# Performance work log

Measured on AMD Instinct MI355X. Metric: run time of the kernel, lower is better.

## Reference

```python
import jax, jax.numpy as jnp
import numpy as np

K = 76          # model dim = 6 + 30 + 30 + 10 (concat of modality embeddings)
H = 8           # heads; per-head dim == K (wide attention variant)
D = 6           # depth
T = 1024        # seq_length (frames)
B = 8           # batch
C = 2           # num_classes
EPS = 1e-5


def setup_inputs() -> dict:
    key = jax.random.key(0)
    ks = jax.random.split(key, 24)
    rn = lambda k, shape, s=0.02: (jax.random.normal(k, shape, jnp.float32) * s)
    return {
        # forward inputs (per-frame multimodal features)
        "v": jax.random.normal(ks[0], (B, T, 6), jnp.float32),
        "x": jax.random.normal(ks[1], (B, T, 137), jnp.float32),
        "y": jax.random.normal(ks[2], (B, T, 113), jnp.float32),
        "z": jax.random.normal(ks[3], (B, T, 35), jnp.float32),
        # modality embed linears (stored (in, out); torch does x @ W.T)
        "W_hp": rn(ks[4], (6, 6)),     "b_hp": jnp.zeros((6,), jnp.float32),
        "W_lm": rn(ks[5], (137, 30)),  "b_lm": jnp.zeros((30,), jnp.float32),
        "W_el": rn(ks[6], (113, 30)),  "b_el": jnp.zeros((30,), jnp.float32),
        "W_au": rn(ks[7], (35, 10)),   "b_au": jnp.zeros((10,), jnp.float32),
        "pos_emb": rn(ks[8], (T, K)),
        # per-block params stacked over depth for lax.scan
        "Wq": rn(ks[9], (D, K, H * K)),
        "Wk": rn(ks[10], (D, K, H * K)),
        "Wv": rn(ks[11], (D, K, H * K)),
        "Wu": rn(ks[12], (D, H * K, K)), "bu": jnp.zeros((D, K), jnp.float32),
        "ln1_s": jnp.ones((D, K), jnp.float32), "ln1_b": jnp.zeros((D, K), jnp.float32),
        "W1": rn(ks[13], (D, K, 4 * K)), "b1": jnp.zeros((D, 4 * K), jnp.float32),
        "W2": rn(ks[14], (D, 4 * K, K)), "b2": jnp.zeros((D, K), jnp.float32),
        "ln2_s": jnp.ones((D, K), jnp.float32), "ln2_b": jnp.zeros((D, K), jnp.float32),
        "W_out": rn(ks[15], (K, C)), "b_out": jnp.zeros((C,), jnp.float32),
    }


def _layernorm(h, s, b):
    mu = jnp.mean(h, axis=-1, keepdims=True)
    var = jnp.mean(jnp.square(h - mu), axis=-1, keepdims=True)
    return (h - mu) * jax.lax.rsqrt(var + EPS) * s + b


def reference(v, x, y, z,
              W_hp, b_hp, W_lm, b_lm, W_el, b_el, W_au, b_au,
              pos_emb, Wq, Wk, Wv, Wu, bu, ln1_s, ln1_b,
              W1, b1, W2, b2, ln2_s, ln2_b, W_out, b_out):
    b, t = v.shape[0], v.shape[1]
    tokens = jnp.concatenate([
        v @ W_hp + b_hp,
        x @ W_lm + b_lm,
        y @ W_el + b_el,
        z @ W_au + b_au,
    ], axis=2)                                   # (b, t, K)
    h = tokens + pos_emb[None, :, :]
    scale = 1.0 / np.sqrt(K)                     # dot / sqrt(e), e == k

    def block(hh, p):
        wq, wk, wv, wu, bu_, l1s, l1b, w1, b1_, w2, b2_, l2s, l2b = p
        # (b, t, H*K) -> (b, H, t, K); per-head dim is full K here
        q = (hh @ wq).reshape(b, t, H, K).transpose(0, 2, 1, 3)
        k_ = (hh @ wk).reshape(b, t, H, K).transpose(0, 2, 1, 3)
        vv = (hh @ wv).reshape(b, t, H, K).transpose(0, 2, 1, 3)
        dot = jax.nn.softmax(jnp.einsum('bhte,bhse->bhts', q, k_) * scale, axis=-1)
        att = jnp.einsum('bhts,bhse->bhte', dot, vv)        # (b, H, t, K)
        att = att.transpose(0, 2, 1, 3).reshape(b, t, H * K)
        att = att @ wu + bu_                                # unify heads -> (b, t, K)
        h1 = _layernorm(att + hh, l1s, l1b)
        ff = jax.nn.relu(h1 @ w1 + b1_) @ w2 + b2_
        return _layernorm(ff + h1, l2s, l2b), None

    h, _ = jax.lax.scan(
        block, h,
        (Wq, Wk, Wv, Wu, bu, ln1_s, ln1_b, W1, b1, W2, b2, ln2_s, ln2_b))
    return h @ W_out + b_out                     # (b, t, num_classes)
```

## Files before the change

### kernel.cpp

```cpp
#include <hip/hip_runtime.h>
#include <hip/hip_bf16.h>
#include <math.h>

#define B_   8
#define T_   1024
#define K_   76
#define KP_  96
#define H_   8
#define D_   6
#define C_   2
#define HK_  608
#define QKLD_ 640
#define FF_  304
#define FFP_ 320
#define EK_  320
#define BT_  8192
#define EPS_ 1e-5f
#define SCL2_ (0.11470786693528088f * 1.4426950408889634f)

typedef unsigned short u16;
typedef unsigned int u32;
typedef short bf16x8 __attribute__((ext_vector_type(8)));
typedef float f32x4 __attribute__((ext_vector_type(4)));

__device__ __forceinline__ u16 f2b(float f) {
  __hip_bfloat16 h = __float2bfloat16(f);
  return *reinterpret_cast<u16*>(&h);
}
__device__ __forceinline__ float b2f(u16 u) {
  __hip_bfloat16 h = *reinterpret_cast<__hip_bfloat16*>(&u);
  return __bfloat162float(h);
}
__device__ __forceinline__ u32 pack2(float a, float b) {
  __hip_bfloat162 t = __float22bfloat162_rn(make_float2(a, b));
  return *reinterpret_cast<u32*>(&t);
}

#define PER_L_ 304128ULL
__global__ __launch_bounds__(256) void wconv_kernel(
    const float* __restrict__ Wq, const float* __restrict__ Wk, const float* __restrict__ Wv,
    const float* __restrict__ Wu, const float* __restrict__ W1, const float* __restrict__ W2,
    u16* __restrict__ WT) {
  __shared__ float Ls[32][65];
  int zz = blockIdx.y;
  int d = zz / 6, wt = zz % 6;
  const float* in; int Kd, Nsrc, Nalloc, Kp; u16* out;
  size_t lb = (size_t)d * PER_L_;
  switch (wt) {
    case 0: in = Wq + (size_t)d*K_*HK_; Kd=K_;  Nsrc=HK_; Nalloc=640; Kp=KP_;  out = WT + lb;          break;
    case 1: in = Wk + (size_t)d*K_*HK_; Kd=K_;  Nsrc=HK_; Nalloc=640; Kp=KP_;  out = WT + lb + 61440;  break;
    case 2: in = Wv + (size_t)d*K_*HK_; Kd=K_;  Nsrc=HK_; Nalloc=640; Kp=KP_;  out = WT + lb + 122880; break;
    case 3: in = Wu + (size_t)d*HK_*K_; Kd=HK_; Nsrc=K_;  Nalloc=96;  Kp=HK_;  out = WT + lb + 184320; break;
    case 4: in = W1 + (size_t)d*K_*FF_; Kd=K_;  Nsrc=FF_; Nalloc=320; Kp=KP_;  out = WT + lb + 242688; break;
    default:in = W2 + (size_t)d*FF_*K_; Kd=FF_; Nsrc=K_;  Nalloc=96;  Kp=FFP_; out = WT + lb + 273408; break;
  }
  int tiles_k = Kp / 32;
  int tiles_n = (Nalloc + 63) / 64;
  int tile = blockIdx.x;
  if (tile >= tiles_k * tiles_n) return;
  int tn = tile / tiles_k, tk = tile % tiles_k;
  int n0 = tn * 64, k0 = tk * 32;
  for (int i = threadIdx.x; i < 2048; i += 256) {
    int kk = i >> 6, nn = i & 63;
    int gk = k0 + kk, gn = n0 + nn;
    int srccol = gn;
    if (wt < 3) {
      int hh8 = gn / 80, ft = gn - hh8 * 80;
      srccol = (ft < 76) ? (hh8 * 76 + ft) : -1;
    }
    Ls[kk][nn] = (gk < Kd && srccol >= 0 && srccol < Nsrc) ? in[(size_t)gk * Nsrc + srccol] : 0.f;
  }
  __syncthreads();
  for (int i = threadIdx.x; i < 2048; i += 256) {
    int nn = i >> 5, kk = i & 31;
    int gn = n0 + nn;
    if (gn < Nalloc) out[(size_t)gn * Kp + k0 + kk] = f2b(Ls[kk][nn]);
  }
}

__global__ void wembed_kernel(const float* __restrict__ W_hp, const float* __restrict__ b_hp,
                              const float* __restrict__ W_lm, const float* __restrict__ b_lm,
                              const float* __restrict__ W_el, const float* __restrict__ b_el,
                              const float* __restrict__ W_au, const float* __restrict__ b_au,
                              u16* __restrict__ WE) {
  int idx = blockIdx.x * 256 + threadIdx.x;
  if (idx >= 96 * EK_) return;
  int n = idx / EK_, kk = idx % EK_;
  float val = 0.f;
  if (n < 76) {
    if (kk < 6) { if (n < 6) val = W_hp[kk * 6 + n]; }
    else if (kk < 143) { int i = kk - 6; if (n >= 6 && n < 36) val = W_lm[i * 30 + (n - 6)]; }
    else if (kk < 256) { int i = kk - 143; if (n >= 36 && n < 66) val = W_el[i * 30 + (n - 36)]; }
    else if (kk < 291) { int i = kk - 256; if (n >= 66) val = W_au[i * 10 + (n - 66)]; }
    else if (kk == 291) {
      val = (n < 6) ? b_hp[n] : (n < 36) ? b_lm[n - 6] : (n < 66) ? b_el[n - 36] : b_au[n - 66];
    }
  }
  WE[idx] = f2b(val);
}

__global__ void pack_kernel(const float* __restrict__ v, const float* __restrict__ x,
                            const float* __restrict__ y, const float* __restrict__ z,
                            u16* __restrict__ xin) {
  int idx = blockIdx.x * 256 + threadIdx.x;
  if (idx >= BT_ * (EK_ / 2)) return;
  int bt = idx / (EK_ / 2), dc = idx % (EK_ / 2);
  int c0 = dc * 2;
  auto fetch = [&](int c) -> float {
    if (c < 6) return v[bt * 6 + c];
    if (c < 143) return x[bt * 137 + c - 6];
    if (c < 256) return y[bt * 113 + c - 143];
    if (c < 291) return z[bt * 35 + c - 256];
    if (c == 291) return 1.0f;
    return 0.f;
  };
  ((u32*)xin)[idx] = pack2(fetch(c0), fetch(c0 + 1));
}

template<int RT, int CT, int KSTEPS, int RELU, int LNFUSE, int TPB>
__global__ __launch_bounds__(TPB) void gemm_kernel(
    const u16* __restrict__ A, int lda,
    const u16* __restrict__ Wt, int ldw, unsigned long long wstride,
    const float* __restrict__ bias,
    u16* __restrict__ Cc, int ldc, int N,
    int ksplit, int klen, unsigned long long osplit,
    float cs,
    u16* __restrict__ vbt,
    const float* __restrict__ pos,
    const u16* __restrict__ res,
    const float* __restrict__ lns,
    const float* __restrict__ lnb) {
  __shared__ u16 Bs[CT * 16 * 56];
  const int tid = threadIdx.x;
  const int w = tid >> 6, lane = tid & 63;
  const int r = lane & 15, g = lane >> 4;
  const int n0 = blockIdx.x * CT * 16;
  const int m0 = blockIdx.y * (TPB / 64) * 16 * RT;
  const int z = blockIdx.z;
  const int k0 = z * ksplit;
  const int kend = k0 + klen;
  const u16* Wz = Wt + (size_t)z * wstride;
  const float* bias_eff = (z == 0) ? bias : nullptr;
  const float csz = (z == 0) ? cs : 1.f;
  u16* Cz = Cc + (size_t)z * osplit;
  constexpr int NB = (CT * 64 + TPB - 1) / TPB;

  const f32x4 fz = {0.f, 0.f, 0.f, 0.f};
  f32x4 acc[RT][CT];
  #pragma unroll
  for (int rt = 0; rt < RT; rt++)
    #pragma unroll
    for (int ct = 0; ct < CT; ct++) acc[rt][ct] = fz;

  bf16x8 a_all[RT][KSTEPS];
  #pragma unroll
  for (int rt = 0; rt < RT; rt++) {
    const u16* arow = A + (size_t)(m0 + (w * RT + rt) * 16 + r) * lda;
    #pragma unroll
    for (int ks = 0; ks < KSTEPS; ks++) {
      int kA = k0 + ks * 32 + g * 8;
      if (kA < kend) a_all[rt][ks] = *(const bf16x8*)(arow + kA);
      else a_all[rt][ks] = bf16x8{0, 0, 0, 0, 0, 0, 0, 0};
    }
  }

  uint4 bpre[NB];
  auto loadB = [&](int ks) {
    int kk = k0 + ks * 32;
    #pragma unroll
    for (int i0 = 0; i0 < NB; i0++) {
      int idx = tid + i0 * TPB;
      bpre[i0] = make_uint4(0, 0, 0, 0);
      if (idx < CT * 64) {
        int nn = idx >> 2, kc = idx & 3;
        if (kk + kc * 8 < kend)
          bpre[i0] = *(const uint4*)(Wz + (size_t)(n0 + nn) * ldw + kk + kc * 8);
      }
    }
  };
  loadB(0);

  for (int ks = 0; ks < KSTEPS; ks++) {
    __syncthreads();
    #pragma unroll
    for (int i0 = 0; i0 < NB; i0++) {
      int idx = tid + i0 * TPB;
      if (idx < CT * 64) {
        int nn = idx >> 2, kc = idx & 3;
        *(uint4*)&Bs[nn * 56 + (((kc ^ (nn & 3)) << 3))] = bpre[i0];
      }
    }
    __syncthreads();
    if (ks + 1 < KSTEPS) loadB(ks + 1);
    #pragma unroll
    for (int ct = 0; ct < CT; ct++) {
      bf16x8 bb = *(const bf16x8*)&Bs[(ct * 16 + r) * 56 + (((g ^ (r & 3)) << 3))];
      #pragma unroll
      for (int rt = 0; rt < RT; rt++)
        acc[rt][ct] = __builtin_amdgcn_mfma_f32_16x16x32_bf16(a_all[rt][ks], bb, acc[rt][ct], 0, 0, 0);
    }
  }

  if (LNFUSE) {
    #pragma unroll
    for (int reg = 0; reg < 4; reg++) {
      int row = m0 + w * 16 + g * 4 + reg;
      const u16* resr = res + (size_t)row * KP_;
      float vals[CT];
      float s = 0.f, s2 = 0.f;
      #pragma unroll
      for (int ct = 0; ct < CT; ct++) {
        int col = ct * 16 + r;
        float val = 0.f;
        if (col < N) {
          val = acc[0][ct][reg] + bias[col] + b2f(resr[col]);
          s += val; s2 += val * val;
        }
        vals[ct] = val;
      }
      #pragma unroll
      for (int m = 1; m < 16; m <<= 1) { s += __shfl_xor(s, m); s2 += __shfl_xor(s2, m); }
      float mu = s * (1.f / 76.f);
      float rstd = rsqrtf(s2 * (1.f / 76.f) - mu * mu + EPS_);
      u16* outr = Cz + (size_t)row * ldc;
      #pragma unroll
      for (int ct = 0; ct < CT; ct++) {
        int col = ct * 16 + r;
        u16 ov = 0;
        if (col < N) ov = f2b((vals[ct] - mu) * rstd * lns[col] + lnb[col]);
        if (col < ldc) outr[col] = ov;
      }
    }
  } else if (vbt && z == 2) {
    #pragma unroll
    for (int rt = 0; rt < RT; rt++) {
      #pragma unroll
      for (int ct = 0; ct < CT; ct++) {
        int feat = ct * 16 + r;
        int token = m0 + (w * RT + rt) * 16 + g * 4;
        int bb_ = token >> 10, tt = token & 1023;
        ushort4 pk;
        if (feat < 76) {
          pk.x = f2b(acc[rt][ct][0]); pk.y = f2b(acc[rt][ct][1]);
          pk.z = f2b(acc[rt][ct][2]); pk.w = f2b(acc[rt][ct][3]);
        } else {
          pk = make_ushort4(0, 0, 0, 0);
        }
        *(ushort4*)(vbt + (((size_t)(bb_ * 8 + blockIdx.x) * 80 + feat) << 10) + tt) = pk;
      }
    }
  } else {
    #pragma unroll
    for (int rt = 0; rt < RT; rt++) {
      #pragma unroll
      for (int ct = 0; ct < CT; ct++) {
        int col = n0 + ct * 16 + r;
        if (col < ldc) {
          #pragma unroll
          for (int reg = 0; reg < 4; reg++) {
            int row = m0 + (w * RT + rt) * 16 + g * 4 + reg;
            float val = acc[rt][ct][reg] * csz;
            if (bias_eff && col < N) val += bias_eff[col];
            if (pos && col < N) val += pos[(row & (T_ - 1)) * K_ + col];
            if (RELU) val = fmaxf(val, 0.f);
            Cz[(size_t)row * ldc + col] = f2b(val);
          }
        }
      }
    }
  }
}

__global__ __launch_bounds__(256, 2) void attn_kernel(const u16* __restrict__ q,
                                                      const u16* __restrict__ k,
                                                      const u16* __restrict__ vbt,
                                                      u16* __restrict__ att) {
  __shared__ u16 Ks[2][64 * 104];
  __shared__ u16 Vs[2][80 * 72];
  __shared__ u32 Psw[128 * 36];
  const int bid = blockIdx.x;
  const int hh = bid & 7, b = (bid >> 3) & 7, qt = bid >> 6;
  const int tid = threadIdx.x;
  const int w = tid >> 6, lane = tid & 63;
  const int r = lane & 15, g = lane >> 4;
  const int qbase = b * T_ + qt * 128;

  bf16x8 aq[2][3];
  #pragma unroll
  for (int rt = 0; rt < 2; rt++) {
    const u16* qsrc = q + (size_t)(qbase + w * 32 + rt * 16 + r) * QKLD_ + hh * 80;
    #pragma unroll
    for (int ks = 0; ks < 3; ks++) {
      int e0 = ks * 32 + g * 8;
      aq[rt][ks] = (e0 < 80) ? *(const bf16x8*)(qsrc + e0) : bf16x8{0, 0, 0, 0, 0, 0, 0, 0};
    }
  }

  const int krow = tid >> 2, kq4 = tid & 3;
  uint4 kpre[3], vpre[3];
  auto stage_load = [&](int kt) {
    const int kb = b * T_ + kt * 64;
    const u16* ksrc = k + (size_t)(kb + krow) * QKLD_ + hh * 80;
    #pragma unroll
    for (int i = 0; i < 3; i++) {
      int c = kq4 + 4 * i;
      kpre[i] = (c < 10) ? *(const uint4*)(ksrc + c * 8) : make_uint4(0, 0, 0, 0);
    }
    const u16* vsrc = vbt + (((size_t)(b * 8 + hh) * 80) << 10) + kt * 64;
    #pragma unroll
    for (int p = 0; p < 3; p++) {
      int idx = tid + p * 256;
      vpre[p] = (idx < 640) ? *(const uint4*)(vsrc + ((size_t)(idx >> 3) << 10) + (idx & 7) * 8)
                            : make_uint4(0, 0, 0, 0);
    }
  };
  auto stage_write = [&](int buf) {
    #pragma unroll
    for (int i = 0; i < 3; i++) {
      int c = kq4 + 4 * i;
      *(uint4*)&Ks[buf][krow * 104 + c * 8] = kpre[i];
    }
    #pragma unroll
    for (int p = 0; p < 3; p++) {
      int idx = tid + p * 256;
      if (idx < 640)
        *(uint4*)&Vs[buf][(idx >> 3) * 72 + (idx & 7) * 8] = vpre[p];
    }
  };

  u32* Pw = Psw + w * 32 * 36;

  const f32x4 fz = {0.f, 0.f, 0.f, 0.f};
  f32x4 o[2][5];
  float ls[2] = {0.f, 0.f};
  #pragma unroll
  for (int rt = 0; rt < 2; rt++)
    #pragma unroll
    for (int i = 0; i < 5; i++) o[rt][i] = fz;

  stage_load(0);
  stage_write(0);
  __syncthreads();

  for (int kt = 0; kt < 16; kt++) {
    const int buf = kt & 1;
    if (kt < 15) stage_load(kt + 1);

    f32x4 st[2][4];
    #pragma unroll
    for (int ct = 0; ct < 4; ct++) { st[0][ct] = fz; st[1][ct] = fz; }
    __builtin_amdgcn_s_setprio(1);
    #pragma unroll
    for (int ct = 0; ct < 4; ct++) {
      #pragma unroll
      for (int ks = 0; ks < 3; ks++) {
        bf16x8 ak = *(const bf16x8*)&Ks[buf][(ct * 16 + r) * 104 + ks * 32 + g * 8];
        st[0][ct] = __builtin_amdgcn_mfma_f32_16x16x32_bf16(ak, aq[0][ks], st[0][ct], 0, 0, 0);
        st[1][ct] = __builtin_amdgcn_mfma_f32_16x16x32_bf16(ak, aq[1][ks], st[1][ct], 0, 0, 0);
      }
    }
    __builtin_amdgcn_s_setprio(0);

    #pragma unroll
    for (int rt = 0; rt < 2; rt++) {
      float rs = 0.f;
      u32 pk[8];
      #pragma unroll
      for (int ct = 0; ct < 4; ct++) {
        float p0 = exp2f(st[rt][ct][0]), p1 = exp2f(st[rt][ct][1]);
        float p2 = exp2f(st[rt][ct][2]), p3 = exp2f(st[rt][ct][3]);
        rs += (p0 + p1) + (p2 + p3);
        pk[ct * 2] = pack2(p0, p1);
        pk[ct * 2 + 1] = pack2(p2, p3);
      }
      rs += __shfl_xor(rs, 16);
      rs += __shfl_xor(rs, 32);
      ls[rt] += rs;
      u32* pw = Pw + (rt * 16 + r) * 36;
      #pragma unroll
      for (int ct = 0; ct < 4; ct++)
        *(uint2*)(pw + ct * 8 + g * 2) = make_uint2(pk[ct * 2], pk[ct * 2 + 1]);
    }

    bf16x8 pa[2][2];
    #pragma unroll
    for (int rt = 0; rt < 2; rt++) {
      const u32* pr = Pw + (rt * 16 + r) * 36;
      #pragma unroll
      for (int ks = 0; ks < 2; ks++) {
        uint4 t = *(const uint4*)(pr + ks * 16 + g * 4);
        pa[rt][ks] = *reinterpret_cast<bf16x8*>(&t);
      }
    }
    __builtin_amdgcn_s_setprio(1);
    #pragma unroll
    for (int ks = 0; ks < 2; ks++) {
      #pragma unroll
      for (int c5 = 0; c5 < 5; c5++) {
        bf16x8 av = *(const bf16x8*)&Vs[buf][(c5 * 16 + r) * 72 + ks * 32 + g * 8];
        #pragma unroll
        for (int rt = 0; rt < 2; rt++)
          o[rt][c5] = __builtin_amdgcn_mfma_f32_16x16x32_bf16(av, pa[rt][ks], o[rt][c5], 0, 0, 0);
      }
    }
    __builtin_amdgcn_s_setprio(0);

    if (kt < 15) stage_write(1 - buf);
    __syncthreads();
  }

  #pragma unroll
  for (int rt = 0; rt < 2; rt++) {
    float inv = 1.f / ls[rt];
    int token = qbase + w * 32 + rt * 16 + r;
    #pragma unroll
    for (int c5 = 0; c5 < 5; c5++) {
      if (c5 == 4 && g == 3) continue;
      ushort4 pk4;
      pk4.x = f2b(o[rt][c5][0] * inv);
      pk4.y = f2b(o[rt][c5][1] * inv);
      pk4.z = f2b(o[rt][c5][2] * inv);
      pk4.w = f2b(o[rt][c5][3] * inv);
      *(ushort4*)&att[(size_t)token * HK_ + hh * 76 + c5 * 16 + g * 4] = pk4;
    }
  }
}

__global__ void out_kernel(const u16* __restrict__ h, const float* __restrict__ W,
                           const float* __restrict__ bias, float* __restrict__ out) {
  int idx = blockIdx.x * 256 + threadIdx.x;
  if (idx >= BT_ * C_) return;
  int bt = idx >> 1, c = idx & 1;
  float acc = bias[c];
  const u16* hr = h + (size_t)bt * KP_;
  #pragma unroll 4
  for (int e = 0; e < K_; e++) acc += b2f(hr[e]) * W[e * C_ + c];
  out[idx] = acc;
}

extern "C" void kernel_launch(void* const* d_in, const int* in_sizes, int n_in,
                              void* d_out, int out_size, void* d_ws, size_t ws_size,
                              hipStream_t stream) {
  const float* v    = (const float*)d_in[0];
  const float* x    = (const float*)d_in[1];
  const float* y    = (const float*)d_in[2];
  const float* z    = (const float*)d_in[3];
  const float* W_hp = (const float*)d_in[4];
  const float* b_hp = (const float*)d_in[5];
  const float* W_lm = (const float*)d_in[6];
  const float* b_lm = (const float*)d_in[7];
  const float* W_el = (const float*)d_in[8];
  const float* b_el = (const float*)d_in[9];
  const float* W_au = (const float*)d_in[10];
  const float* b_au = (const float*)d_in[11];
  const float* pos  = (const float*)d_in[12];
  const float* Wq   = (const float*)d_in[13];
  const float* Wk   = (const float*)d_in[14];
  const float* Wv   = (const float*)d_in[15];
  const float* Wu   = (const float*)d_in[16];
  const float* bu   = (const float*)d_in[17];
  const float* ln1s = (const float*)d_in[18];
  const float* ln1b = (const float*)d_in[19];
  const float* W1   = (const float*)d_in[20];
  const float* b1   = (const float*)d_in[21];
  const float* W2   = (const float*)d_in[22];
  const float* b2   = (const float*)d_in[23];
  const float* ln2s = (const float*)d_in[24];
  const float* ln2b = (const float*)d_in[25];
  const float* Wout = (const float*)d_in[26];
  const float* bout = (const float*)d_in[27];

  u16* ws  = (u16*)d_ws;
  u16* WT  = ws;
  u16* WE  = WT + 1824768;
  u16* h   = WE + 30720;
  u16* xin = h + 786432;
  u16* qb  = xin + 2621440;
  u16* kb  = qb + 5242880;
  u16* vbt = kb + 5242880;
  u16* att = vbt + 5242880;
  u16* h1  = kb;
  u16* ff  = att;

  wconv_kernel<<<dim3(38, 36), 256, 0, stream>>>(Wq, Wk, Wv, Wu, W1, W2, WT);
  wembed_kernel<<<(96 * EK_ + 255) / 256, 256, 0, stream>>>(
      W_hp, b_hp, W_lm, b_lm, W_el, b_el, W_au, b_au, WE);
  pack_kernel<<<(BT_ * (EK_ / 2) + 255) / 256, 256, 0, stream>>>(v, x, y, z, xin);
  gemm_kernel<1, 6, 10, 0, 0, 128><<<dim3(1, 256, 1), 128, 0, stream>>>(
      xin, EK_, WE, EK_, 0ULL, nullptr, h, KP_, K_, 0, EK_, 0ULL,
      1.f, nullptr, pos, nullptr, nullptr, nullptr);

  for (int d = 0; d < D_; d++) {
    u16* WTd = WT + (size_t)d * PER_L_;
    const float* bu_d = bu + (size_t)d * K_;
    const float* l1s  = ln1s + (size_t)d * K_;
    const float* l1b  = ln1b + (size_t)d * K_;
    const float* b1_d = b1 + (size_t)d * FF_;
    const float* b2_d = b2 + (size_t)d * K_;
    const float* l2s  = ln2s + (size_t)d * K_;
    const float* l2b  = ln2b + (size_t)d * K_;

    gemm_kernel<2, 5, 3, 0, 0, 256><<<dim3(8, 64, 3), 256, 0, stream>>>(
        h, KP_, WTd, KP_, 61440ULL, nullptr, qb, QKLD_, QKLD_, 0, KP_, 5242880ULL,
        SCL2_, vbt, nullptr, nullptr, nullptr, nullptr);
    attn_kernel<<<dim3(512), 256, 0, stream>>>(qb, kb, vbt, att);
    gemm_kernel<1, 6, 19, 0, 1, 128><<<dim3(1, 256, 1), 128, 0, stream>>>(
        att, HK_, WTd + 184320, HK_, 0ULL, bu_d, h1, KP_, K_, 0, HK_, 0ULL,
        1.f, nullptr, nullptr, h, l1s, l1b);
    gemm_kernel<2, 5, 3, 1, 0, 256><<<dim3(4, 64, 1), 256, 0, stream>>>(
        h1, KP_, WTd + 242688, KP_, 0ULL, b1_d, ff, FFP_, FF_, 0, KP_, 0ULL,
        1.f, nullptr, nullptr, nullptr, nullptr, nullptr);
    gemm_kernel<1, 6, 10, 0, 1, 128><<<dim3(1, 256, 1), 128, 0, stream>>>(
        ff, FFP_, WTd + 273408, FFP_, 0ULL, b2_d, h, KP_, K_, 0, FFP_, 0ULL,
        1.f, nullptr, nullptr, h1, l2s, l2b);
  }

  out_kernel<<<(BT_ * C_ + 255) / 256, 256, 0, stream>>>(h, Wout, bout, (float*)d_out);
}
```

Baseline: 641.9 us.

## Split attention block into eight waves of sixteen query rows each

The attention kernel goes from 256 to 512 threads per block. Each wave now owns 16 query rows instead of 32, which halves the per-wave score, output and Q fragment registers. The K/V staging is remapped so 512 threads cover the 64-row K tile and the 640-chunk V tile. The aim is more resident waves per CU to hide LDS and exp latency, at the cost of each K/V LDS fragment feeding only one MFMA instead of two, so LDS read traffic per FLOP doubles.

Result: no change. 644.5 us (+0.4%).

```diff
diff --git a/kernel.cpp b/kernel.cpp
--- a/kernel.cpp
+++ b/kernel.cpp
@@ -271,7 +271,7 @@
   }
 }
 
-__global__ __launch_bounds__(256, 2) void attn_kernel(const u16* __restrict__ q,
+__global__ __launch_bounds__(512, 4) void attn_kernel(const u16* __restrict__ q,
                                                       const u16* __restrict__ k,
                                                       const u16* __restrict__ vbt,
                                                       u16* __restrict__ att) {
@@ -285,58 +285,42 @@
   const int r = lane & 15, g = lane >> 4;
   const int qbase = b * T_ + qt * 128;
 
-  bf16x8 aq[2][3];
-  #pragma unroll
-  for (int rt = 0; rt < 2; rt++) {
-    const u16* qsrc = q + (size_t)(qbase + w * 32 + rt * 16 + r) * QKLD_ + hh * 80;
+  bf16x8 aq[3];
+  {
+    const u16* qsrc = q + (size_t)(qbase + w * 16 + r) * QKLD_ + hh * 80;
     #pragma unroll
     for (int ks = 0; ks < 3; ks++) {
       int e0 = ks * 32 + g * 8;
-      aq[rt][ks] = (e0 < 80) ? *(const bf16x8*)(qsrc + e0) : bf16x8{0, 0, 0, 0, 0, 0, 0, 0};
-    }
-  }
-
-  const int krow = tid >> 2, kq4 = tid & 3;
-  uint4 kpre[3], vpre[3];
+      aq[ks] = (e0 < 80) ? *(const bf16x8*)(qsrc + e0) : bf16x8{0, 0, 0, 0, 0, 0, 0, 0};
+    }
+  }
+
+  const int krow = tid >> 3, kc8 = tid & 7;
+  uint4 kpreA, kpreB, vpreA, vpreB;
   auto stage_load = [&](int kt) {
     const int kb = b * T_ + kt * 64;
     const u16* ksrc = k + (size_t)(kb + krow) * QKLD_ + hh * 80;
-    #pragma unroll
-    for (int i = 0; i < 3; i++) {
-      int c = kq4 + 4 * i;
-      kpre[i] = (c < 10) ? *(const uint4*)(ksrc + c * 8) : make_uint4(0, 0, 0, 0);
-    }
+    kpreA = *(const uint4*)(ksrc + kc8 * 8);
+    kpreB = (kc8 < 2) ? *(const uint4*)(ksrc + (8 + kc8) * 8) : make_uint4(0, 0, 0, 0);
     const u16* vsrc = vbt + (((size_t)(b * 8 + hh) * 80) << 10) + kt * 64;
-    #pragma unroll
-    for (int p = 0; p < 3; p++) {
-      int idx = tid + p * 256;
-      vpre[p] = (idx < 640) ? *(const uint4*)(vsrc + ((size_t)(idx >> 3) << 10) + (idx & 7) * 8)
-                            : make_uint4(0, 0, 0, 0);
-    }
+    vpreA = *(const uint4*)(vsrc + ((size_t)(tid >> 3) << 10) + (tid & 7) * 8);
+    if (tid < 128)
+      vpreB = *(const uint4*)(vsrc + ((size_t)((512 + tid) >> 3) << 10) + (tid & 7) * 8);
   };
   auto stage_write = [&](int buf) {
-    #pragma unroll
-    for (int i = 0; i < 3; i++) {
-      int c = kq4 + 4 * i;
-      *(uint4*)&Ks[buf][krow * 104 + c * 8] = kpre[i];
-    }
-    #pragma unroll
-    for (int p = 0; p < 3; p++) {
-      int idx = tid + p * 256;
-      if (idx < 640)
-        *(uint4*)&Vs[buf][(idx >> 3) * 72 + (idx & 7) * 8] = vpre[p];
-    }
+    *(uint4*)&Ks[buf][krow * 104 + kc8 * 8] = kpreA;
+    if (kc8 < 4) *(uint4*)&Ks[buf][krow * 104 + (8 + kc8) * 8] = kpreB;
+    *(uint4*)&Vs[buf][(tid >> 3) * 72 + (tid & 7) * 8] = vpreA;
+    if (tid < 128) *(uint4*)&Vs[buf][((512 + tid) >> 3) * 72 + (tid & 7) * 8] = vpreB;
   };
 
-  u32* Pw = Psw + w * 32 * 36;
+  u32* Pw = Psw + w * 16 * 36;
 
   const f32x4 fz = {0.f, 0.f, 0.f, 0.f};
-  f32x4 o[2][5];
-  float ls[2] = {0.f, 0.f};
+  f32x4 o[5];
+  float ls = 0.f;
   #pragma unroll
-  for (int rt = 0; rt < 2; rt++)
-    #pragma unroll
-    for (int i = 0; i < 5; i++) o[rt][i] = fz;
+  for (int i = 0; i < 5; i++) o[i] = fz;
 
   stage_load(0);
   stage_write(0);
@@ -346,50 +330,47 @@
     const int buf = kt & 1;
     if (kt < 15) stage_load(kt + 1);
 
-    f32x4 st[2][4];
-    #pragma unroll
-    for (int ct = 0; ct < 4; ct++) { st[0][ct] = fz; st[1][ct] = fz; }
+    f32x4 st[4];
+    #pragma unroll
+    for (int ct = 0; ct < 4; ct++) st[ct] = fz;
     __builtin_amdgcn_s_setprio(1);
     #pragma unroll
     for (int ct = 0; ct < 4; ct++) {
       #pragma unroll
       for (int ks = 0; ks < 3; ks++) {
         bf16x8 ak = *(const bf16x8*)&Ks[buf][(ct * 16 + r) * 104 + ks * 32 + g * 8];
-        st[0][ct] = __builtin_amdgcn_mfma_f32_16x16x32_bf16(ak, aq[0][ks], st[0][ct], 0, 0, 0);
-        st[1][ct] = __builtin_amdgcn_mfma_f32_16x16x32_bf16(ak, aq[1][ks], st[1][ct], 0, 0, 0);
+        st[ct] = __builtin_amdgcn_mfma_f32_16x16x32_bf16(ak, aq[ks], st[ct], 0, 0, 0);
       }
     }
     __builtin_amdgcn_s_setprio(0);
 
-    #pragma unroll
-    for (int rt = 0; rt < 2; rt++) {
+    {
       float rs = 0.f;
       u32 pk[8];
       #pragma unroll
       for (int ct = 0; ct < 4; ct++) {
-        float p0 = exp2f(st[rt][ct][0]), p1 = exp2f(st[rt][ct][1]);
-        float p2 = exp2f(st[rt][ct][2]), p3 = exp2f(st[rt][ct][3]);
+        float p0 = exp2f(st[ct][0]), p1 = exp2f(st[ct][1]);
+        float p2 = exp2f(st[ct][2]), p3 = exp2f(st[ct][3]);
         rs += (p0 + p1) + (p2 + p3);
         pk[ct * 2] = pack2(p0, p1);
         pk[ct * 2 + 1] = pack2(p2, p3);
       }
       rs += __shfl_xor(rs, 16);
       rs += __shfl_xor(rs, 32);
-      ls[rt] += rs;
-      u32* pw = Pw + (rt * 16 + r) * 36;
+      ls += rs;
+      u32* pw = Pw + r * 36;
       #pragma unroll
       for (int ct = 0; ct < 4; ct++)
         *(uint2*)(pw + ct * 8 + g * 2) = make_uint2(pk[ct * 2], pk[ct * 2 + 1]);
     }
 
-    bf16x8 pa[2][2];
-    #pragma unroll
-    for (int rt = 0; rt < 2; rt++) {
-      const u32* pr = Pw + (rt * 16 + r) * 36;
+    bf16x8 pa[2];
+    {
+      const u32* pr = Pw + r * 36;
       #pragma unroll
       for (int ks = 0; ks < 2; ks++) {
         uint4 t = *(const uint4*)(pr + ks * 16 + g * 4);
-        pa[rt][ks] = *reinterpret_cast<bf16x8*>(&t);
+        pa[ks] = *reinterpret_cast<bf16x8*>(&t);
       }
     }
     __builtin_amdgcn_s_setprio(1);
@@ -398,9 +379,7 @@
       #pragma unroll
       for (int c5 = 0; c5 < 5; c5++) {
         bf16x8 av = *(const bf16x8*)&Vs[buf][(c5 * 16 + r) * 72 + ks * 32 + g * 8];
-        #pragma unroll
-        for (int rt = 0; rt < 2; rt++)
-          o[rt][c5] = __builtin_amdgcn_mfma_f32_16x16x32_bf16(av, pa[rt][ks], o[rt][c5], 0, 0, 0);
+        o[c5] = __builtin_amdgcn_mfma_f32_16x16x32_bf16(av, pa[ks], o[c5], 0, 0, 0);
       }
     }
     __builtin_amdgcn_s_setprio(0);
@@ -409,18 +388,17 @@
     __syncthreads();
   }
 
-  #pragma unroll
-  for (int rt = 0; rt < 2; rt++) {
-    float inv = 1.f / ls[rt];
-    int token = qbase + w * 32 + rt * 16 + r;
+  {
+    float inv = 1.f / ls;
+    int token = qbase + w * 16 + r;
     #pragma unroll
     for (int c5 = 0; c5 < 5; c5++) {
       if (c5 == 4 && g == 3) continue;
       ushort4 pk4;
-      pk4.x = f2b(o[rt][c5][0] * inv);
-      pk4.y = f2b(o[rt][c5][1] * inv);
-      pk4.z = f2b(o[rt][c5][2] * inv);
-      pk4.w = f2b(o[rt][c5][3] * inv);
+      pk4.x = f2b(o[c5][0] * inv);
+      pk4.y = f2b(o[c5][1] * inv);
+      pk4.z = f2b(o[c5][2] * inv);
+      pk4.w = f2b(o[c5][3] * inv);
       *(ushort4*)&att[(size_t)token * HK_ + hh * 76 + c5 * 16 + g * 4] = pk4;
     }
   }
@@ -503,7 +481,7 @@
     gemm_kernel<2, 5, 3, 0, 0, 256><<<dim3(8, 64, 3), 256, 0, stream>>>(
         h, KP_, WTd, KP_, 61440ULL, nullptr, qb, QKLD_, QKLD_, 0, KP_, 5242880ULL,
         SCL2_, vbt, nullptr, nullptr, nullptr, nullptr);
-    attn_kernel<<<dim3(512), 256, 0, stream>>>(qb, kb, vbt, att);
+    attn_kernel<<<dim3(512), 512, 0, stream>>>(qb, kb, vbt, att);
     gemm_kernel<1, 6, 19, 0, 1, 128><<<dim3(1, 256, 1), 128, 0, stream>>>(
         att, HK_, WTd + 184320, HK_, 0ULL, bu_d, h1, KP_, K_, 0, HK_, 0ULL,
         1.f, nullptr, nullptr, h, l1s, l1b);
```

## Single-buffer attention LDS for higher occupancy, defer row-sum reduction, vectorize out kernel

Applied to the files above, without the earlier changes.

The attention kernel drops its double-buffered K/V shared-memory tiles for single buffers and raises the launch-bounds occupancy target from 2 to 3 blocks per CU. Global loads are still prefetched into registers, but each iteration now needs two barriers around the LDS write. The per-tile cross-lane shuffles for the softmax row sum are moved to one reduction after the loop. The output projection now has each thread compute both classes from packed bf16 pairs, halving the thread count.

Result: no change. 641.4 us (-0.1%).

```diff
diff --git a/kernel.cpp b/kernel.cpp
--- a/kernel.cpp
+++ b/kernel.cpp
@@ -271,12 +271,12 @@
   }
 }
 
-__global__ __launch_bounds__(256, 2) void attn_kernel(const u16* __restrict__ q,
+__global__ __launch_bounds__(256, 3) void attn_kernel(const u16* __restrict__ q,
                                                       const u16* __restrict__ k,
                                                       const u16* __restrict__ vbt,
                                                       u16* __restrict__ att) {
-  __shared__ u16 Ks[2][64 * 104];
-  __shared__ u16 Vs[2][80 * 72];
+  __shared__ u16 Ks[64 * 104];
+  __shared__ u16 Vs[80 * 72];
   __shared__ u32 Psw[128 * 36];
   const int bid = blockIdx.x;
   const int hh = bid & 7, b = (bid >> 3) & 7, qt = bid >> 6;
@@ -314,17 +314,17 @@
                             : make_uint4(0, 0, 0, 0);
     }
   };
-  auto stage_write = [&](int buf) {
+  auto stage_write = [&]() {
     #pragma unroll
     for (int i = 0; i < 3; i++) {
       int c = kq4 + 4 * i;
-      *(uint4*)&Ks[buf][krow * 104 + c * 8] = kpre[i];
+      *(uint4*)&Ks[krow * 104 + c * 8] = kpre[i];
     }
     #pragma unroll
     for (int p = 0; p < 3; p++) {
       int idx = tid + p * 256;
       if (idx < 640)
-        *(uint4*)&Vs[buf][(idx >> 3) * 72 + (idx & 7) * 8] = vpre[p];
+        *(uint4*)&Vs[(idx >> 3) * 72 + (idx & 7) * 8] = vpre[p];
     }
   };
 
@@ -339,11 +339,11 @@
     for (int i = 0; i < 5; i++) o[rt][i] = fz;
 
   stage_load(0);
-  stage_write(0);
-  __syncthreads();
 
   for (int kt = 0; kt < 16; kt++) {
-    const int buf = kt & 1;
+    __syncthreads();
+    stage_write();
+    __syncthreads();
     if (kt < 15) stage_load(kt + 1);
 
     f32x4 st[2][4];
@@ -354,7 +354,7 @@
     for (int ct = 0; ct < 4; ct++) {
       #pragma unroll
       for (int ks = 0; ks < 3; ks++) {
-        bf16x8 ak = *(const bf16x8*)&Ks[buf][(ct * 16 + r) * 104 + ks * 32 + g * 8];
+        bf16x8 ak = *(const bf16x8*)&Ks[(ct * 16 + r) * 104 + ks * 32 + g * 8];
         st[0][ct] = __builtin_amdgcn_mfma_f32_16x16x32_bf16(ak, aq[0][ks], st[0][ct], 0, 0, 0);
         st[1][ct] = __builtin_amdgcn_mfma_f32_16x16x32_bf16(ak, aq[1][ks], st[1][ct], 0, 0, 0);
       }
@@ -373,8 +373,6 @@
         pk[ct * 2] = pack2(p0, p1);
         pk[ct * 2 + 1] = pack2(p2, p3);
       }
-      rs += __shfl_xor(rs, 16);
-      rs += __shfl_xor(rs, 32);
       ls[rt] += rs;
       u32* pw = Pw + (rt * 16 + r) * 36;
       #pragma unroll
@@ -397,20 +395,19 @@
     for (int ks = 0; ks < 2; ks++) {
       #pragma unroll
       for (int c5 = 0; c5 < 5; c5++) {
-        bf16x8 av = *(const bf16x8*)&Vs[buf][(c5 * 16 + r) * 72 + ks * 32 + g * 8];
+        bf16x8 av = *(const bf16x8*)&Vs[(c5 * 16 + r) * 72 + ks * 32 + g * 8];
         #pragma unroll
         for (int rt = 0; rt < 2; rt++)
           o[rt][c5] = __builtin_amdgcn_mfma_f32_16x16x32_bf16(av, pa[rt][ks], o[rt][c5], 0, 0, 0);
       }
     }
     __builtin_amdgcn_s_setprio(0);
-
-    if (kt < 15) stage_write(1 - buf);
-    __syncthreads();
   }
 
   #pragma unroll
   for (int rt = 0; rt < 2; rt++) {
+    ls[rt] += __shfl_xor(ls[rt], 16);
+    ls[rt] += __shfl_xor(ls[rt], 32);
     float inv = 1.f / ls[rt];
     int token = qbase + w * 32 + rt * 16 + r;
     #pragma unroll
@@ -428,14 +425,19 @@
 
 __global__ void out_kernel(const u16* __restrict__ h, const float* __restrict__ W,
                            const float* __restrict__ bias, float* __restrict__ out) {
-  int idx = blockIdx.x * 256 + threadIdx.x;
-  if (idx >= BT_ * C_) return;
-  int bt = idx >> 1, c = idx & 1;
-  float acc = bias[c];
-  const u16* hr = h + (size_t)bt * KP_;
+  int bt = blockIdx.x * 256 + threadIdx.x;
+  if (bt >= BT_) return;
+  const u32* hr = (const u32*)(h + (size_t)bt * KP_);
+  float acc0 = bias[0], acc1 = bias[1];
   #pragma unroll 4
-  for (int e = 0; e < K_; e++) acc += b2f(hr[e]) * W[e * C_ + c];
-  out[idx] = acc;
+  for (int d = 0; d < 38; d++) {
+    u32 h2 = hr[d];
+    float f0 = b2f((u16)(h2 & 0xffff)), f1 = b2f((u16)(h2 >> 16));
+    acc0 += f0 * W[(2 * d) * 2] + f1 * W[(2 * d + 1) * 2];
+    acc1 += f0 * W[(2 * d) * 2 + 1] + f1 * W[(2 * d + 1) * 2 + 1];
+  }
+  out[bt * 2] = acc0;
+  out[bt * 2 + 1] = acc1;
 }
 
 extern "C" void kernel_launch(void* const* d_in, const int* in_sizes, int n_in,
@@ -515,5 +517,5 @@
         1.f, nullptr, nullptr, h1, l2s, l2b);
   }
 
-  out_kernel<<<(BT_ * C_ + 255) / 256, 256, 0, stream>>>(h, Wout, bout, (float*)d_out);
-}
+  out_kernel<<<(BT_ + 255) / 256, 256, 0, stream>>>(h, Wout, bout, (float*)d_out);
+}
```
